# Optimization experiments

Hardware: AMD Instinct MI355X
Metric: run time of the kernel (lower is better)

The kernel has to match this reference:

```python
import jax, jax.numpy as jnp
import numpy as np

B, S, D, H = 4, 2048, 1024, 16
HD = D // H  # head_dim = 64


def setup_inputs() -> dict:
    key = jax.random.key(0)
    ks = jax.random.split(key, 7)
    sc = 0.02
    return {
        "data": jax.random.normal(ks[0], (B, S, D), jnp.float32),
        "context": jax.random.normal(ks[1], (B, S, D), jnp.float32),
        "Wq": jax.random.normal(ks[2], (D, D), jnp.float32) * sc,
        "bq": jnp.zeros((D,), jnp.float32),
        "Wk": jax.random.normal(ks[3], (D, D), jnp.float32) * sc,
        "bk": jnp.zeros((D,), jnp.float32),
        "Wv": jax.random.normal(ks[4], (D, D), jnp.float32) * sc,
        "bv": jnp.zeros((D,), jnp.float32),
        "Wo": jax.random.normal(ks[5], (D, D), jnp.float32) * sc,
        "bo": jnp.zeros((D,), jnp.float32),
    }


def reference(data, context, Wq, bq, Wk, bk, Wv, bv, Wo, bo):
    # Projections (torch Linear: x @ W.T + b; here W stored as [in, out])
    Q = data @ Wq + bq          # [B,S,D]
    K = context @ Wk + bk
    V = context @ Wv + bv
    # split heads -> [B,H,S,HD]
    Q = Q.reshape(B, S, H, HD).transpose(0, 2, 1, 3)
    K = K.reshape(B, S, H, HD).transpose(0, 2, 1, 3)
    V = V.reshape(B, S, H, HD).transpose(0, 2, 1, 3)
    scale = jnp.sqrt(jnp.asarray(HD, Q.dtype))
    scores = jnp.einsum("bhqd,bhkd->bhqk", Q, K) / scale  # [B,H,S,S]
    causal = jnp.tril(jnp.ones((S, S), bool))              # row >= col
    scores = jnp.where(causal[None, None], scores, jnp.asarray(-jnp.inf, scores.dtype))
    probs = jax.nn.softmax(scores, axis=-1)
    Z = jnp.einsum("bhqk,bhkd->bhqd", probs, V)            # [B,H,S,HD]
    Z = Z.transpose(0, 2, 1, 3).reshape(B, S, D)
    return Z @ Wo + bo
```

## Files before the change

kernel.cpp:

```cpp
#include <hip/hip_runtime.h>

#define B_  4
#define S_  2048
#define D_  1024
#define H_  16
#define HD_ 64
#define M_  (B_*S_)

typedef _Float16 f16;
typedef f16  f16x8 __attribute__((ext_vector_type(8)));
typedef f16  f16x4 __attribute__((ext_vector_type(4)));
typedef float f32x4 __attribute__((ext_vector_type(4)));

__device__ __forceinline__ void gload_lds16(const f16* g, f16* l) {
    __builtin_amdgcn_global_load_lds(
        (const __attribute__((address_space(1))) void*)g,
        (__attribute__((address_space(3))) void*)l, 16, 0, 0);
}

__global__ __launch_bounds__(256) void cvt2_kernel(const float* __restrict__ a,
                                                   const float* __restrict__ c,
                                                   f16* __restrict__ out, int n4each) {
    int i = blockIdx.x * 256 + threadIdx.x;
    const float* src = (i < n4each) ? a : c;
    int j = (i < n4each) ? i : i - n4each;
    f32x4 v = *reinterpret_cast<const f32x4*>(src + (size_t)j * 4);
    *reinterpret_cast<f16x4*>(out + (size_t)i * 4) = __builtin_convertvector(v, f16x4);
}

__global__ __launch_bounds__(256) void transpose_cvt4_kernel(const float* __restrict__ Wq,
                                                             const float* __restrict__ Wk,
                                                             const float* __restrict__ Wv,
                                                             const float* __restrict__ Wo,
                                                             f16* __restrict__ WT) {
    __shared__ float tile[32][33];
    const int z = blockIdx.z;
    const float* W = (z == 0) ? Wq : (z == 1) ? Wk : (z == 2) ? Wv : Wo;
    f16* dst = WT + (size_t)z * D_ * D_;
    const int n0 = blockIdx.x * 32, k0 = blockIdx.y * 32;
    const int tx = threadIdx.x & 31, ty = threadIdx.x >> 5;
#pragma unroll
    for (int j = 0; j < 4; ++j)
        tile[ty + 8 * j][tx] = W[(size_t)(k0 + ty + 8 * j) * D_ + n0 + tx];
    __syncthreads();
#pragma unroll
    for (int j = 0; j < 4; ++j)
        dst[(size_t)(n0 + ty + 8 * j) * D_ + k0 + tx] = (f16)tile[tx][ty + 8 * j];
}

template <int MODE>
__global__ __launch_bounds__(512) void gemm8(const f16* __restrict__ Adata,
                                             const f16* __restrict__ Actx,
                                             const f16* __restrict__ Wt,
                                             const float* __restrict__ bq,
                                             const float* __restrict__ bk,
                                             const float* __restrict__ bv,
                                             f16* __restrict__ Qb,
                                             f16* __restrict__ Kb,
                                             f16* __restrict__ VtB,
                                             float* __restrict__ Cout) {
    extern __shared__ __align__(16) f16 SM[];
    constexpr int K = D_;
    constexpr int NT = K / 64;
    constexpr int NXT = (MODE == 0) ? 12 : 4;
    constexpr int PER = (MODE == 0) ? 96 : 32;
    const int id = (int)blockIdx.x;
    const int work = (id & 7) * PER + (id >> 3);
    const int wy = work / NXT, wx = work - wy * NXT;
    const int seg = (MODE == 0) ? (wx >> 2) : 0;
    const f16* __restrict__ A = (MODE == 0) ? (seg ? Actx : Adata) : Adata;
    const int m0 = wy * 128, n0 = wx * 256;
    const int tid = (int)threadIdx.x;
    const int w = tid >> 6, lr = tid & 15, lg = (tid & 63) >> 4;
    const int wr = w >> 1, wc = w & 1;
    const int swx = lr & 7;
    const int srow = tid >> 3;
    const int g16 = (tid & 7) ^ (srow & 7);

    auto stageA = [&](int kt, int buf) {
        const f16* src = A + (size_t)(m0 + srow) * K + kt * 64 + g16 * 8;
        f16* dst = SM + buf * 8192;
        gload_lds16(src, dst + w * 512);
        gload_lds16(src + (size_t)64 * K, dst + 4096 + w * 512);
    };
    auto stageB = [&](int kt, int buf, int h) {
        const f16* src = Wt + (size_t)(n0 + h * 128 + srow) * K + kt * 64 + g16 * 8;
        f16* dst = SM + 16384 + buf * 16384 + h * 8192;
        gload_lds16(src, dst + w * 512);
        gload_lds16(src + (size_t)64 * K, dst + 4096 + w * 512);
    };
    auto LDA = [&](int buf, int m, int kk) -> f16x8 {
        return *reinterpret_cast<const f16x8*>(
            SM + buf * 8192 + (wr * 32 + m * 16 + lr) * 64 + (((kk * 4 + lg) ^ swx) * 8));
    };
    auto LDB = [&](int buf, int n, int kk) -> f16x8 {
        return *reinterpret_cast<const f16x8*>(
            SM + 16384 + buf * 16384 + wc * 8192 + (n * 16 + lr) * 64 + (((kk * 4 + lg) ^ swx) * 8));
    };

    f32x4 acc[2][8] = {};
    stageA(0, 0); stageB(0, 0, 0); stageB(0, 0, 1); stageA(1, 1);
    asm volatile("s_waitcnt vmcnt(2)" ::: "memory");
    __builtin_amdgcn_s_barrier();

    for (int t = 0; t < NT; ++t) {
        const int buf = t & 1, nb = buf ^ 1;
        f16x8 a[2][2], b[2][2];
#pragma unroll
        for (int m = 0; m < 2; ++m) { a[m][0] = LDA(buf, m, 0); a[m][1] = LDA(buf, m, 1); }
        b[0][0] = LDB(buf, 0, 0); b[0][1] = LDB(buf, 0, 1);
        b[1][0] = LDB(buf, 1, 0); b[1][1] = LDB(buf, 1, 1);
        f16x8 b2[2][2];
        b2[0][0] = LDB(buf, 2, 0); b2[0][1] = LDB(buf, 2, 1);
        b2[1][0] = LDB(buf, 3, 0); b2[1][1] = LDB(buf, 3, 1);
        if (t + 1 < NT) { stageB(t + 1, nb, 0); stageB(t + 1, nb, 1); }
        else { asm volatile("s_waitcnt vmcnt(0)" ::: "memory"); }
        __builtin_amdgcn_s_barrier();
        __builtin_amdgcn_s_setprio(1);
#pragma unroll
        for (int kk = 0; kk < 2; ++kk)
#pragma unroll
            for (int m = 0; m < 2; ++m) {
                acc[m][0] = __builtin_amdgcn_mfma_f32_16x16x32_f16(a[m][kk], b[0][kk], acc[m][0], 0, 0, 0);
                acc[m][1] = __builtin_amdgcn_mfma_f32_16x16x32_f16(a[m][kk], b[1][kk], acc[m][1], 0, 0, 0);
                acc[m][2] = __builtin_amdgcn_mfma_f32_16x16x32_f16(a[m][kk], b2[0][kk], acc[m][2], 0, 0, 0);
                acc[m][3] = __builtin_amdgcn_mfma_f32_16x16x32_f16(a[m][kk], b2[1][kk], acc[m][3], 0, 0, 0);
            }
        __builtin_amdgcn_s_setprio(0);
        __builtin_amdgcn_s_barrier();
        b[0][0] = LDB(buf, 4, 0); b[0][1] = LDB(buf, 4, 1);
        b[1][0] = LDB(buf, 5, 0); b[1][1] = LDB(buf, 5, 1);
        b2[0][0] = LDB(buf, 6, 0); b2[0][1] = LDB(buf, 6, 1);
        b2[1][0] = LDB(buf, 7, 0); b2[1][1] = LDB(buf, 7, 1);
        if (t + 2 < NT) stageA(t + 2, buf);
        if (t + 1 < NT) { asm volatile("s_waitcnt vmcnt(2)" ::: "memory"); }
        __builtin_amdgcn_s_barrier();
        __builtin_amdgcn_s_setprio(1);
#pragma unroll
        for (int kk = 0; kk < 2; ++kk)
#pragma unroll
            for (int m = 0; m < 2; ++m) {
                acc[m][4] = __builtin_amdgcn_mfma_f32_16x16x32_f16(a[m][kk], b[0][kk], acc[m][4], 0, 0, 0);
                acc[m][5] = __builtin_amdgcn_mfma_f32_16x16x32_f16(a[m][kk], b[1][kk], acc[m][5], 0, 0, 0);
                acc[m][6] = __builtin_amdgcn_mfma_f32_16x16x32_f16(a[m][kk], b2[0][kk], acc[m][6], 0, 0, 0);
                acc[m][7] = __builtin_amdgcn_mfma_f32_16x16x32_f16(a[m][kk], b2[1][kk], acc[m][7], 0, 0, 0);
            }
        __builtin_amdgcn_s_setprio(0);
        __builtin_amdgcn_s_barrier();
    }
    if (MODE == 1) {
        const float* bias = bq;
#pragma unroll
        for (int n = 0; n < 8; ++n) {
            const int col = n0 + wc * 128 + n * 16 + lr;
            const float bvv = bias[col];
#pragma unroll
            for (int m = 0; m < 2; ++m) {
                const int row = m0 + wr * 32 + m * 16 + lg * 4;
#pragma unroll
                for (int r = 0; r < 4; ++r)
                    Cout[(size_t)(row + r) * D_ + col] = acc[m][n][r] + bvv;
            }
        }
    } else {
        const float* bias = (seg == 0) ? bq : (seg == 1) ? bk : bv;
#pragma unroll
        for (int n = 0; n < 8; ++n) {
            const int col = n0 + wc * 128 + n * 16 + lr;
            const int lc = col & 1023;
            const float bvv = bias[lc];
#pragma unroll
            for (int m = 0; m < 2; ++m) {
                const int row = m0 + wr * 32 + m * 16 + lg * 4;
                if (seg == 2) {
                    const int bb = row >> 11, s0 = row & 2047;
                    f16x4 v;
#pragma unroll
                    for (int r = 0; r < 4; ++r) v[r] = (f16)(acc[m][n][r] + bvv);
                    *reinterpret_cast<f16x4*>(VtB + ((size_t)(bb * D_ + lc)) * S_ + s0) = v;
                } else {
                    f16* dst = seg ? Kb : Qb;
#pragma unroll
                    for (int r = 0; r < 4; ++r)
                        dst[(size_t)(row + r) * D_ + lc] = (f16)(acc[m][n][r] + bvv);
                }
            }
        }
    }
}

__global__ __launch_bounds__(256, 2) void attn_kernel(const f16* __restrict__ Q,
                                                      const f16* __restrict__ Kg,
                                                      const f16* __restrict__ Vt,
                                                      f16* __restrict__ Z) {
    __shared__ __align__(16) f16 KL[2][64 * 64];
    __shared__ __align__(16) f16 VL[2][64 * 64];
    __shared__ __align__(16) f16 Pl[4][32][72];
    const int h = blockIdx.x, b = blockIdx.y, pp = blockIdx.z;
    const int tid = threadIdx.x, w = tid >> 6, l = tid & 63, lr = l & 15, lg = l >> 4;
    const size_t base   = ((size_t)b * S_) * D_ + h * HD_;
    const size_t vtbase = ((size_t)(b * D_ + h * HD_)) * S_;
    const f16* __restrict__ Kbase = Kg + base;
    const f16* __restrict__ Vbase = Vt + vtbase;
    const float sc = 0.125f * 1.44269504f;
    const int sw_xor = lr & 7;
    f16x8 onesv;
#pragma unroll
    for (int i = 0; i < 8; ++i) onesv[i] = (f16)1.0f;

    auto stageKV = [&](int buf, int t0) {
#pragma unroll
        for (int i = 0; i < 2; ++i) {
            const int c = i * 256 + tid;
            const int row = c >> 3, g16 = (c & 7) ^ (row & 7);
            f16* dstK = &KL[buf][(i * 256 + w * 64) * 8];
            f16* dstV = &VL[buf][(i * 256 + w * 64) * 8];
            gload_lds16(Kbase + (size_t)(t0 + row) * D_ + g16 * 8, dstK);
            gload_lds16(Vbase + (size_t)row * S_ + t0 + g16 * 8, dstV);
        }
    };

    for (int half = 0; half < 2; ++half) {
        const int qt = half ? pp : (15 - pp);
        const int q0 = qt * 128, wq0 = q0 + w * 32;
        const int ntw = ((wq0 + 31) >> 6) + 1;
        const int ntb = qt * 2 + 2;

        f16x8 qf[2][2];
#pragma unroll
        for (int mf = 0; mf < 2; ++mf)
#pragma unroll
            for (int kd = 0; kd < 2; ++kd)
                qf[mf][kd] = *reinterpret_cast<const f16x8*>(
                    Q + base + (size_t)(wq0 + mf * 16 + lr) * D_ + kd * 32 + lg * 8);

        f32x4 zacc[2][4] = {};
        f32x4 lsv[2] = {};
        float mrun[2] = {-3.0e38f, -3.0e38f};

        stageKV(0, 0);
        for (int t = 0; t < ntb; ++t) {
            const int buf = t & 1;
            if (t + 1 < ntb) {
                stageKV(buf ^ 1, (t + 1) * 64);
                asm volatile("s_waitcnt vmcnt(4)" ::: "memory");
            } else {
                asm volatile("s_waitcnt vmcnt(0)" ::: "memory");
            }
            __builtin_amdgcn_s_barrier();
            if (t < ntw) {
                const int t0 = t * 64;
                f16x8 kf[2][4];
#pragma unroll
                for (int kd = 0; kd < 2; ++kd)
#pragma unroll
                    for (int n = 0; n < 4; ++n)
                        kf[kd][n] = *reinterpret_cast<const f16x8*>(
                            &KL[buf][(n * 16 + lr) * 64 + (((kd * 4 + lg) ^ sw_xor) * 8)]);
                f32x4 sf[2][4] = {};
                __builtin_amdgcn_s_setprio(1);
#pragma unroll
                for (int kd = 0; kd < 2; ++kd)
#pragma unroll
                    for (int n = 0; n < 4; ++n)
#pragma unroll
                        for (int mf = 0; mf < 2; ++mf)
                            sf[mf][n] = __builtin_amdgcn_mfma_f32_16x16x32_f16(kf[kd][n], qf[mf][kd], sf[mf][n], 0, 0, 0);
                __builtin_amdgcn_s_setprio(0);
                f16x8 vf[2][4];
#pragma unroll
                for (int kt = 0; kt < 2; ++kt)
#pragma unroll
                    for (int n = 0; n < 4; ++n)
                        vf[kt][n] = *reinterpret_cast<const f16x8*>(
                            &VL[buf][(n * 16 + lr) * 64 + (((kt * 4 + lg) ^ sw_xor) * 8)]);
                if (t == ntw - 1) {
#pragma unroll
                    for (int mf = 0; mf < 2; ++mf)
#pragma unroll
                        for (int n = 0; n < 4; ++n)
#pragma unroll
                            for (int r = 0; r < 4; ++r)
                                if ((t0 + n * 16 + lg * 4 + r) > (wq0 + mf * 16 + lr))
                                    sf[mf][n][r] = -3.0e38f;
                }
#pragma unroll
                for (int mf = 0; mf < 2; ++mf) {
                    f32x4 t4;
#pragma unroll
                    for (int r = 0; r < 4; ++r)
                        t4[r] = fmaxf(fmaxf(sf[mf][0][r], sf[mf][1][r]), fmaxf(sf[mf][2][r], sf[mf][3][r]));
                    float vmax = fmaxf(fmaxf(t4[0], t4[1]), fmaxf(t4[2], t4[3]));
                    vmax = fmaxf(vmax, __shfl_xor(vmax, 16));
                    vmax = fmaxf(vmax, __shfl_xor(vmax, 32));
                    const float vs = vmax * sc;
                    const bool norm = !__all(vs <= mrun[mf] + 10.0f);
                    if (norm) {
                        const float mnew = fmaxf(mrun[mf], vs);
                        const float al = __builtin_amdgcn_exp2f(mrun[mf] - mnew);
                        mrun[mf] = mnew;
#pragma unroll
                        for (int r = 0; r < 4; ++r) {
                            const float ar = __shfl(al, lg * 4 + r);
#pragma unroll
                            for (int n = 0; n < 4; ++n) zacc[mf][n][r] *= ar;
                            lsv[mf][r] *= ar;
                        }
                    }
#pragma unroll
                    for (int n = 0; n < 4; ++n) {
                        f32x4 p;
#pragma unroll
                        for (int r = 0; r < 4; ++r)
                            p[r] = __builtin_amdgcn_exp2f(fmaf(sf[mf][n][r], sc, -mrun[mf]));
                        f16x4 pv;
#pragma unroll
                        for (int r = 0; r < 4; ++r) pv[r] = (f16)p[r];
                        *reinterpret_cast<f16x4*>(&Pl[w][mf * 16 + lr][n * 16 + lg * 4]) = pv;
                    }
                }
#pragma unroll
                for (int kt = 0; kt < 2; ++kt) {
                    f16x8 pa[2];
#pragma unroll
                    for (int mf = 0; mf < 2; ++mf)
                        pa[mf] = *reinterpret_cast<const f16x8*>(&Pl[w][mf * 16 + lr][kt * 32 + lg * 8]);
                    __builtin_amdgcn_s_setprio(1);
#pragma unroll
                    for (int n = 0; n < 4; ++n)
#pragma unroll
                        for (int mf = 0; mf < 2; ++mf)
                            zacc[mf][n] = __builtin_amdgcn_mfma_f32_16x16x32_f16(pa[mf], vf[kt][n], zacc[mf][n], 0, 0, 0);
#pragma unroll
                    for (int mf = 0; mf < 2; ++mf)
                        lsv[mf] = __builtin_amdgcn_mfma_f32_16x16x32_f16(pa[mf], onesv, lsv[mf], 0, 0, 0);
                    __builtin_amdgcn_s_setprio(0);
                }
            }
            __builtin_amdgcn_s_barrier();
        }
#pragma unroll
        for (int mf = 0; mf < 2; ++mf) {
            f32x4 inv;
#pragma unroll
            for (int r = 0; r < 4; ++r) inv[r] = 1.0f / lsv[mf][r];
#pragma unroll
            for (int r = 0; r < 4; ++r)
#pragma unroll
                for (int n = 0; n < 4; ++n)
                    Z[base + (size_t)(wq0 + mf * 16 + lg * 4 + r) * D_ + n * 16 + lr] =
                        (f16)(zacc[mf][n][r] * inv[r]);
        }
    }
}

extern "C" void kernel_launch(void* const* d_in, const int* in_sizes, int n_in,
                              void* d_out, int out_size, void* d_ws, size_t ws_size,
                              hipStream_t stream) {
    const float* data    = (const float*)d_in[0];
    const float* context = (const float*)d_in[1];
    const float* Wq = (const float*)d_in[2];
    const float* bq = (const float*)d_in[3];
    const float* Wk = (const float*)d_in[4];
    const float* bk = (const float*)d_in[5];
    const float* Wv = (const float*)d_in[6];
    const float* bv = (const float*)d_in[7];
    const float* Wo = (const float*)d_in[8];
    const float* bo = (const float*)d_in[9];

    const size_t MD = (size_t)M_ * D_;
    const size_t DD = (size_t)D_ * D_;
    f16* dataB = (f16*)d_ws;
    f16* ctxB  = dataB + MD;
    f16* WqT   = ctxB + MD;
    f16* WkT   = WqT + DD;
    f16* WvT   = WkT + DD;
    f16* WoT   = WvT + DD;
    f16* Qb    = WoT + DD;
    f16* Kb    = Qb + MD;
    f16* VtB   = Kb + MD;
    f16* Zb    = VtB + MD;

    (void)WkT; (void)WvT;

    const int n4 = (int)(MD / 4);
    cvt2_kernel<<<2 * n4 / 256, 256, 0, stream>>>(data, context, dataB, n4);
    transpose_cvt4_kernel<<<dim3(32, 32, 4), 256, 0, stream>>>(Wq, Wk, Wv, Wo, WqT);

    hipFuncSetAttribute(reinterpret_cast<const void*>(gemm8<0>),
                        hipFuncAttributeMaxDynamicSharedMemorySize, 98304);
    hipFuncSetAttribute(reinterpret_cast<const void*>(gemm8<1>),
                        hipFuncAttributeMaxDynamicSharedMemorySize, 98304);

    gemm8<0><<<768, 512, 98304, stream>>>(dataB, ctxB, WqT, bq, bk, bv,
                                          Qb, Kb, VtB, nullptr);

    attn_kernel<<<dim3(H_, B_, 8), 256, 0, stream>>>(Qb, Kb, VtB, Zb);

    gemm8<1><<<256, 512, 98304, stream>>>(Zb, nullptr, WoT, bo, nullptr, nullptr,
                                          nullptr, nullptr, nullptr, (float*)d_out);
}
```

Baseline: 178.4 us.

## Restructure projection GEMMs to 4 warps, triple-buffered BK=32 pipeline

The projection and output GEMMs are rewritten to use 256 threads (4 waves) per 128x256 tile instead of 512 threads. Each wave now computes a 64x128 sub-tile with 32 accumulators. The K loop now uses 32-wide steps with a three-stage LDS ring, loading two tiles ahead, and one barrier per iteration in place of the earlier split-half double-buffer schedule. The aim is fewer barriers, more MFMA work per LDS read and more latency hiding. The cost is higher register pressure (128 accumulator floats per thread), and launch_bounds(256,2) may force spills.

Measured after the change: 170.8 us. -4.3%, faster.

```diff
diff --git a/kernel.cpp b/kernel.cpp
--- a/kernel.cpp
+++ b/kernel.cpp
@@ -49,19 +49,19 @@
 }
 
 template <int MODE>
-__global__ __launch_bounds__(512) void gemm8(const f16* __restrict__ Adata,
-                                             const f16* __restrict__ Actx,
-                                             const f16* __restrict__ Wt,
-                                             const float* __restrict__ bq,
-                                             const float* __restrict__ bk,
-                                             const float* __restrict__ bv,
-                                             f16* __restrict__ Qb,
-                                             f16* __restrict__ Kb,
-                                             f16* __restrict__ VtB,
-                                             float* __restrict__ Cout) {
+__global__ __launch_bounds__(256, 2) void gemm3p(const f16* __restrict__ Adata,
+                                                 const f16* __restrict__ Actx,
+                                                 const f16* __restrict__ Wt,
+                                                 const float* __restrict__ b0,
+                                                 const float* __restrict__ b1,
+                                                 const float* __restrict__ b2,
+                                                 f16* __restrict__ Qb,
+                                                 f16* __restrict__ Kb,
+                                                 f16* __restrict__ VtB,
+                                                 float* __restrict__ Cout) {
     extern __shared__ __align__(16) f16 SM[];
     constexpr int K = D_;
-    constexpr int NT = K / 64;
+    constexpr int NT = K / 32;
     constexpr int NXT = (MODE == 0) ? 12 : 4;
     constexpr int PER = (MODE == 0) ? 96 : 32;
     const int id = (int)blockIdx.x;
@@ -73,105 +73,92 @@
     const int tid = (int)threadIdx.x;
     const int w = tid >> 6, lr = tid & 15, lg = (tid & 63) >> 4;
     const int wr = w >> 1, wc = w & 1;
-    const int swx = lr & 7;
-    const int srow = tid >> 3;
-    const int g16 = (tid & 7) ^ (srow & 7);
-
-    auto stageA = [&](int kt, int buf) {
-        const f16* src = A + (size_t)(m0 + srow) * K + kt * 64 + g16 * 8;
-        f16* dst = SM + buf * 8192;
-        gload_lds16(src, dst + w * 512);
-        gload_lds16(src + (size_t)64 * K, dst + 4096 + w * 512);
+    const int sw = (lr >> 1) & 3;
+
+    auto stage = [&](int buf, int kt) {
+        const int kk0 = kt * 32;
+        f16* base = SM + buf * 12288;
+#pragma unroll
+        for (int j = 0; j < 2; ++j) {
+            const int c = j * 256 + tid;
+            const int row = c >> 2;
+            const int ks = ((c & 3) ^ ((row >> 1) & 3)) * 8;
+            gload_lds16(A + (size_t)(m0 + row) * K + kk0 + ks,
+                        base + (j * 256 + w * 64) * 8);
+        }
+#pragma unroll
+        for (int j = 0; j < 4; ++j) {
+            const int c = j * 256 + tid;
+            const int row = c >> 2;
+            const int ks = ((c & 3) ^ ((row >> 1) & 3)) * 8;
+            gload_lds16(Wt + (size_t)(n0 + row) * K + kk0 + ks,
+                        base + 4096 + (j * 256 + w * 64) * 8);
+        }
     };
-    auto stageB = [&](int kt, int buf, int h) {
-        const f16* src = Wt + (size_t)(n0 + h * 128 + srow) * K + kt * 64 + g16 * 8;
-        f16* dst = SM + 16384 + buf * 16384 + h * 8192;
-        gload_lds16(src, dst + w * 512);
-        gload_lds16(src + (size_t)64 * K, dst + 4096 + w * 512);
+    auto LDA = [&](int buf, int m) -> f16x8 {
+        return *reinterpret_cast<const f16x8*>(
+            SM + buf * 12288 + (wr * 64 + m * 16 + lr) * 32 + ((lg ^ sw) * 8));
     };
-    auto LDA = [&](int buf, int m, int kk) -> f16x8 {
+    auto LDB = [&](int buf, int n) -> f16x8 {
         return *reinterpret_cast<const f16x8*>(
-            SM + buf * 8192 + (wr * 32 + m * 16 + lr) * 64 + (((kk * 4 + lg) ^ swx) * 8));
+            SM + buf * 12288 + 4096 + (wc * 128 + n * 16 + lr) * 32 + ((lg ^ sw) * 8));
     };
-    auto LDB = [&](int buf, int n, int kk) -> f16x8 {
-        return *reinterpret_cast<const f16x8*>(
-            SM + 16384 + buf * 16384 + wc * 8192 + (n * 16 + lr) * 64 + (((kk * 4 + lg) ^ swx) * 8));
-    };
-
-    f32x4 acc[2][8] = {};
-    stageA(0, 0); stageB(0, 0, 0); stageB(0, 0, 1); stageA(1, 1);
-    asm volatile("s_waitcnt vmcnt(2)" ::: "memory");
+
+    f32x4 acc[4][8] = {};
+    stage(0, 0);
+    stage(1, 1);
+    asm volatile("s_waitcnt vmcnt(6)" ::: "memory");
     __builtin_amdgcn_s_barrier();
 
+    int buf = 0;
     for (int t = 0; t < NT; ++t) {
-        const int buf = t & 1, nb = buf ^ 1;
-        f16x8 a[2][2], b[2][2];
-#pragma unroll
-        for (int m = 0; m < 2; ++m) { a[m][0] = LDA(buf, m, 0); a[m][1] = LDA(buf, m, 1); }
-        b[0][0] = LDB(buf, 0, 0); b[0][1] = LDB(buf, 0, 1);
-        b[1][0] = LDB(buf, 1, 0); b[1][1] = LDB(buf, 1, 1);
-        f16x8 b2[2][2];
-        b2[0][0] = LDB(buf, 2, 0); b2[0][1] = LDB(buf, 2, 1);
-        b2[1][0] = LDB(buf, 3, 0); b2[1][1] = LDB(buf, 3, 1);
-        if (t + 1 < NT) { stageB(t + 1, nb, 0); stageB(t + 1, nb, 1); }
-        else { asm volatile("s_waitcnt vmcnt(0)" ::: "memory"); }
+        if (t + 2 < NT) {
+            int nb = buf + 2; if (nb >= 3) nb -= 3;
+            stage(nb, t + 2);
+        }
+        f16x8 a[4], b[8];
+#pragma unroll
+        for (int m = 0; m < 4; ++m) a[m] = LDA(buf, m);
+#pragma unroll
+        for (int n = 0; n < 8; ++n) b[n] = LDB(buf, n);
+        __builtin_amdgcn_s_setprio(1);
+#pragma unroll
+        for (int m = 0; m < 4; ++m)
+#pragma unroll
+            for (int n = 0; n < 8; ++n)
+                acc[m][n] = __builtin_amdgcn_mfma_f32_16x16x32_f16(a[m], b[n], acc[m][n], 0, 0, 0);
+        __builtin_amdgcn_s_setprio(0);
+        if (t + 2 < NT) {
+            asm volatile("s_waitcnt vmcnt(6)" ::: "memory");
+        } else if (t + 1 < NT) {
+            asm volatile("s_waitcnt vmcnt(0)" ::: "memory");
+        }
         __builtin_amdgcn_s_barrier();
-        __builtin_amdgcn_s_setprio(1);
-#pragma unroll
-        for (int kk = 0; kk < 2; ++kk)
-#pragma unroll
-            for (int m = 0; m < 2; ++m) {
-                acc[m][0] = __builtin_amdgcn_mfma_f32_16x16x32_f16(a[m][kk], b[0][kk], acc[m][0], 0, 0, 0);
-                acc[m][1] = __builtin_amdgcn_mfma_f32_16x16x32_f16(a[m][kk], b[1][kk], acc[m][1], 0, 0, 0);
-                acc[m][2] = __builtin_amdgcn_mfma_f32_16x16x32_f16(a[m][kk], b2[0][kk], acc[m][2], 0, 0, 0);
-                acc[m][3] = __builtin_amdgcn_mfma_f32_16x16x32_f16(a[m][kk], b2[1][kk], acc[m][3], 0, 0, 0);
-            }
-        __builtin_amdgcn_s_setprio(0);
-        __builtin_amdgcn_s_barrier();
-        b[0][0] = LDB(buf, 4, 0); b[0][1] = LDB(buf, 4, 1);
-        b[1][0] = LDB(buf, 5, 0); b[1][1] = LDB(buf, 5, 1);
-        b2[0][0] = LDB(buf, 6, 0); b2[0][1] = LDB(buf, 6, 1);
-        b2[1][0] = LDB(buf, 7, 0); b2[1][1] = LDB(buf, 7, 1);
-        if (t + 2 < NT) stageA(t + 2, buf);
-        if (t + 1 < NT) { asm volatile("s_waitcnt vmcnt(2)" ::: "memory"); }
-        __builtin_amdgcn_s_barrier();
-        __builtin_amdgcn_s_setprio(1);
-#pragma unroll
-        for (int kk = 0; kk < 2; ++kk)
-#pragma unroll
-            for (int m = 0; m < 2; ++m) {
-                acc[m][4] = __builtin_amdgcn_mfma_f32_16x16x32_f16(a[m][kk], b[0][kk], acc[m][4], 0, 0, 0);
-                acc[m][5] = __builtin_amdgcn_mfma_f32_16x16x32_f16(a[m][kk], b[1][kk], acc[m][5], 0, 0, 0);
-                acc[m][6] = __builtin_amdgcn_mfma_f32_16x16x32_f16(a[m][kk], b2[0][kk], acc[m][6], 0, 0, 0);
-                acc[m][7] = __builtin_amdgcn_mfma_f32_16x16x32_f16(a[m][kk], b2[1][kk], acc[m][7], 0, 0, 0);
-            }
-        __builtin_amdgcn_s_setprio(0);
-        __builtin_amdgcn_s_barrier();
+        if (++buf >= 3) buf = 0;
     }
     if (MODE == 1) {
-        const float* bias = bq;
 #pragma unroll
         for (int n = 0; n < 8; ++n) {
             const int col = n0 + wc * 128 + n * 16 + lr;
-            const float bvv = bias[col];
-#pragma unroll
-            for (int m = 0; m < 2; ++m) {
-                const int row = m0 + wr * 32 + m * 16 + lg * 4;
+            const float bvv = b0[col];
+#pragma unroll
+            for (int m = 0; m < 4; ++m) {
+                const int row = m0 + wr * 64 + m * 16 + lg * 4;
 #pragma unroll
                 for (int r = 0; r < 4; ++r)
                     Cout[(size_t)(row + r) * D_ + col] = acc[m][n][r] + bvv;
             }
         }
     } else {
-        const float* bias = (seg == 0) ? bq : (seg == 1) ? bk : bv;
+        const float* bias = (seg == 0) ? b0 : (seg == 1) ? b1 : b2;
 #pragma unroll
         for (int n = 0; n < 8; ++n) {
             const int col = n0 + wc * 128 + n * 16 + lr;
             const int lc = col & 1023;
             const float bvv = bias[lc];
 #pragma unroll
-            for (int m = 0; m < 2; ++m) {
-                const int row = m0 + wr * 32 + m * 16 + lg * 4;
+            for (int m = 0; m < 4; ++m) {
+                const int row = m0 + wr * 64 + m * 16 + lg * 4;
                 if (seg == 2) {
                     const int bb = row >> 11, s0 = row & 2047;
                     f16x4 v;
@@ -387,16 +374,16 @@
     cvt2_kernel<<<2 * n4 / 256, 256, 0, stream>>>(data, context, dataB, n4);
     transpose_cvt4_kernel<<<dim3(32, 32, 4), 256, 0, stream>>>(Wq, Wk, Wv, Wo, WqT);
 
-    hipFuncSetAttribute(reinterpret_cast<const void*>(gemm8<0>),
-                        hipFuncAttributeMaxDynamicSharedMemorySize, 98304);
-    hipFuncSetAttribute(reinterpret_cast<const void*>(gemm8<1>),
-                        hipFuncAttributeMaxDynamicSharedMemorySize, 98304);
-
-    gemm8<0><<<768, 512, 98304, stream>>>(dataB, ctxB, WqT, bq, bk, bv,
-                                          Qb, Kb, VtB, nullptr);
+    hipFuncSetAttribute(reinterpret_cast<const void*>(gemm3p<0>),
+                        hipFuncAttributeMaxDynamicSharedMemorySize, 73728);
+    hipFuncSetAttribute(reinterpret_cast<const void*>(gemm3p<1>),
+                        hipFuncAttributeMaxDynamicSharedMemorySize, 73728);
+
+    gemm3p<0><<<768, 256, 73728, stream>>>(dataB, ctxB, WqT, bq, bk, bv,
+                                           Qb, Kb, VtB, nullptr);
 
     attn_kernel<<<dim3(H_, B_, 8), 256, 0, stream>>>(Qb, Kb, VtB, Zb);
 
-    gemm8<1><<<256, 512, 98304, stream>>>(Zb, nullptr, WoT, bo, nullptr, nullptr,
-                                          nullptr, nullptr, nullptr, (float*)d_out);
-}
+    gemm3p<1><<<256, 256, 73728, stream>>>(Zb, nullptr, WoT, bo, nullptr, nullptr,
+                                           nullptr, nullptr, nullptr, (float*)d_out);
+}
```
